# Kernel tuning notes

Measured on AMD Instinct MI355X. Metric: run time of the kernel, lower is better.

Reference implementation:

```python
import jax, jax.numpy as jnp
import numpy as np

HEADS = 4
ALPHA = 0.2
NEG = -9.0e15


def _layer(h, adj_mask, W, linW, linb, qkvW, qkvb, a, concat):
    # One GraphSelfAttentionLayer (eval mode: dropout off).
    F_out = W.shape[-1]
    n = h.shape[0]
    Wh = (h @ W) @ linW + linb                      # [N, F]
    qkv = Wh @ qkvW + qkvb                          # [N, 3F]
    q, k, v = jnp.split(qkv, 3, axis=-1)
    to_heads = lambda t: t.reshape(n, HEADS, F_out // HEADS).transpose(1, 0, 2)
    q, k, v = to_heads(q), to_heads(k), to_heads(v)  # [H, N, d]
    # note: scale uses out_features (not per-head d), matching the source
    dots = jax.nn.softmax(jnp.einsum('hid,hjd->hij', q, k) * (F_out ** -0.5), axis=-1)
    Wh0 = jnp.einsum('hij,hjd->hid', dots, v).transpose(1, 0, 2).reshape(n, F_out)
    Wh0 = jax.nn.softmax(Wh0, axis=-1)
    # decomposed all-pairs GAT score: e[i,j] = leakyrelu(Wh_i.a1 + Wh_j.a2)
    f1 = Wh @ a[:F_out]                             # [N]
    f2 = Wh @ a[F_out:]
    e = jax.nn.leaky_relu(f1[:, None] + f2[None, :], ALPHA)
    logits = jnp.where(adj_mask, e + dots.sum(0), NEG)
    att = jax.nn.softmax(logits, axis=1)
    hp = att @ Wh + Wh0
    return jax.nn.elu(hp) if concat else hp


def setup_inputs() -> dict:
    key = jax.random.key(0)
    ks = jax.random.split(key, 16)
    N, NFEAT, NHID, NOUT, H = 3072, 128, 32, 64, 4
    s = 0.1
    return {
        'x': jax.random.normal(ks[0], (N, NFEAT), jnp.float32),
        'adj': jax.random.randint(ks[1], (N, N), 0, 2, dtype=jnp.int32),
        'W_h': jax.random.normal(ks[2], (H, NFEAT, NHID), jnp.float32) * s,
        'lin_W_h': jax.random.normal(ks[3], (H, NHID, NHID), jnp.float32) * s,
        'lin_b_h': jax.random.normal(ks[4], (H, NHID), jnp.float32) * s,
        'qkv_W_h': jax.random.normal(ks[5], (H, NHID, 3 * NHID), jnp.float32) * s,
        'qkv_b_h': jax.random.normal(ks[6], (H, 3 * NHID), jnp.float32) * s,
        'a_h': jax.random.normal(ks[7], (H, 2 * NHID), jnp.float32) * s,
        'W_o': jax.random.normal(ks[8], (NHID * H, NOUT), jnp.float32) * s,
        'lin_W_o': jax.random.normal(ks[9], (NOUT, NOUT), jnp.float32) * s,
        'lin_b_o': jax.random.normal(ks[10], (NOUT,), jnp.float32) * s,
        'qkv_W_o': jax.random.normal(ks[11], (NOUT, 3 * NOUT), jnp.float32) * s,
        'qkv_b_o': jax.random.normal(ks[12], (3 * NOUT,), jnp.float32) * s,
        'a_o': jax.random.normal(ks[13], (2 * NOUT,), jnp.float32) * s,
    }


def reference(x, adj, W_h, lin_W_h, lin_b_h, qkv_W_h, qkv_b_h, a_h,
              W_o, lin_W_o, lin_b_o, qkv_W_o, qkv_b_o, a_o):
    mask = adj > 0
    heads_out = jax.vmap(
        lambda W, lW, lb, qW, qb, a: _layer(x, mask, W, lW, lb, qW, qb, a, True)
    )(W_h, lin_W_h, lin_b_h, qkv_W_h, qkv_b_h, a_h)      # [H, N, NHID]
    n = x.shape[0]
    x1 = jax.nn.elu(heads_out.transpose(1, 0, 2).reshape(n, -1))  # cat(dim=1) then elu
    out = jax.nn.elu(_layer(x1, mask, W_o, lin_W_o, lin_b_o, qkv_W_o, qkv_b_o, a_o, False))
    return out
```

## Files before the change

kernel.cpp:

```cpp
#include <hip/hip_runtime.h>
#include <hip/hip_bf16.h>

#define LOG2E 1.4426950408889634f
#define DEFER_THR 11.0f

typedef unsigned int u32;
typedef float f32x16 __attribute__((ext_vector_type(16)));
typedef short sh8 __attribute__((ext_vector_type(8)));

union FR { u32 u[4]; sh8 s; };

__device__ __forceinline__ u32 cvt_pk_bf16(float lo, float hi){
  u32 r;
  asm volatile("v_cvt_pk_bf16_f32 %0, %1, %2" : "=v"(r) : "v"(lo), "v"(hi));
  return r;
}

template<int W>
__device__ __forceinline__ float wred_max(float v){
  #pragma unroll
  for (int o=1;o<W;o<<=1) v = fmaxf(v, __shfl_xor(v,o));
  return v;
}
template<int W>
__device__ __forceinline__ float wred_sum(float v){
  #pragma unroll
  for (int o=1;o<W;o<<=1) v += __shfl_xor(v,o);
  return v;
}

__global__ __launch_bounds__(256) void k_mask(const int* __restrict__ adj, u32* __restrict__ mk){
  int id = blockIdx.x*256 + threadIdx.x;
  const int4* src = (const int4*)(adj + (size_t)id*32);
  u32 m = 0;
  #pragma unroll
  for (int g=0; g<8; g++){
    int4 v = src[g];
    if (v.x>0) m |= 1u<<(g*4+0);
    if (v.y>0) m |= 1u<<(g*4+1);
    if (v.z>0) m |= 1u<<(g*4+2);
    if (v.w>0) m |= 1u<<(g*4+3);
  }
  mk[id] = m;
}

template<int FIN, int F>
__global__ __launch_bounds__(256) void k_pre_a(const float* __restrict__ xg, const float* __restrict__ Wg,
    const float* __restrict__ lWg, const float* __restrict__ lbg, float* __restrict__ Whg, int N)
{
  const int h = blockIdx.y;
  const int row = blockIdx.x*256 + threadIdx.x;
  __shared__ float Wl[FIN*F];
  __shared__ float lWl[F*F];
  __shared__ float lbl[F];
  for (int i=threadIdx.x;i<FIN*F;i+=256) Wl[i]=Wg[(size_t)h*FIN*F+i];
  for (int i=threadIdx.x;i<F*F;i+=256) lWl[i]=lWg[(size_t)h*F*F+i];
  if (threadIdx.x<F) lbl[threadIdx.x]=lbg[h*F+threadIdx.x];
  __syncthreads();
  float t[F];
  #pragma unroll
  for (int c=0;c<F;c++) t[c]=0.f;
  const float4* xr = (const float4*)(xg + (size_t)row*FIN);
  for (int k4=0;k4<FIN/4;k4++){
    float4 xv = xr[k4];
    float xs[4]={xv.x,xv.y,xv.z,xv.w};
    #pragma unroll
    for (int kk=0;kk<4;kk++){
      float x1 = xs[kk];
      const float* wrow = Wl + (k4*4+kk)*F;
      #pragma unroll
      for (int c=0;c<F;c++) t[c] = fmaf(x1, wrow[c], t[c]);
    }
  }
  float wh[F];
  #pragma unroll
  for (int c=0;c<F;c++) wh[c]=lbl[c];
  #pragma unroll
  for (int k=0;k<F;k++){
    float tv=t[k];
    #pragma unroll
    for (int c=0;c<F;c++) wh[c]=fmaf(tv, lWl[k*F+c], wh[c]);
  }
  float4* dst=(float4*)(Whg + ((size_t)h*N+row)*F);
  #pragma unroll
  for (int c4=0;c4<F/4;c4++) dst[c4]=make_float4(wh[c4*4],wh[c4*4+1],wh[c4*4+2],wh[c4*4+3]);
}

template<int F, int GPR>
__global__ __launch_bounds__(256) void k_pre_b(const float* __restrict__ Whg, const float* __restrict__ qWg,
   const float* __restrict__ qbg, const float* __restrict__ ag,
   float* __restrict__ qg, float* __restrict__ kg, float* __restrict__ vg,
   float* __restrict__ f1g, float* __restrict__ f2g, int N)
{
  constexpr int ROWS = 256/GPR;
  constexpr int GC3  = 3*F/GPR;
  const int h = blockIdx.y;
  const int rl = threadIdx.x / GPR, grp = threadIdx.x % GPR;
  const int row = blockIdx.x*ROWS + rl;
  __shared__ float qWl[F*3*F];
  __shared__ float qbl[3*F];
  __shared__ float al[2*F];
  __shared__ float whl[ROWS][F+1];
  for (int i=threadIdx.x;i<F*3*F;i+=256) qWl[i]=qWg[(size_t)h*F*3*F+i];
  if (threadIdx.x<3*F) qbl[threadIdx.x]=qbg[h*3*F+threadIdx.x];
  if (threadIdx.x<2*F) al[threadIdx.x]=ag[h*2*F+threadIdx.x];
  {
    const float4* wsrc = (const float4*)(Whg + ((size_t)h*N+row)*F);
    #pragma unroll
    for (int c4=0;c4<2;c4++){
      float4 t = wsrc[grp*2+c4];
      int b = grp*8+c4*4;
      whl[rl][b]=t.x; whl[rl][b+1]=t.y; whl[rl][b+2]=t.z; whl[rl][b+3]=t.w;
    }
  }
  __syncthreads();
  float acc[GC3];
  #pragma unroll
  for (int c=0;c<GC3;c++) acc[c]=qbl[grp*GC3+c];
  for (int k=0;k<F;k++){
    float wv = whl[rl][k];
    #pragma unroll
    for (int c=0;c<GC3;c++) acc[c]=fmaf(wv, qWl[k*3*F + grp*GC3 + c], acc[c]);
  }
  size_t base = ((size_t)h*N+row)*F;
  #pragma unroll
  for (int c=0;c<GC3;c++){
    int col = grp*GC3+c;
    if (col < F)        qg[base+col]       = acc[c];
    else if (col < 2*F) kg[base+col-F]     = acc[c];
    else                vg[base+col-2*F]   = acc[c];
  }
  if (grp<2){
    const float* av = al + grp*F;
    float s=0.f;
    for (int k=0;k<F;k++) s = fmaf(whl[rl][k], av[k], s);
    (grp? f2g:f1g)[(size_t)h*N+row] = s;
  }
}

template<int S>
__global__ __launch_bounds__(256) void k_sweep1_mfma32(const float* __restrict__ qg, const float* __restrict__ kg,
    const float* __restrict__ vg, float* __restrict__ pml, float* __restrict__ pw, int N, float qscale)
{
  constexpr int F=32, LROW=33;
  const int h = blockIdx.z;
  const int sc = blockIdx.y;
  const int JC = N/S;
  const int wid = threadIdx.x>>6;
  const int lane = threadIdx.x&63;
  const int l31 = lane&31;
  const int half = lane>>5;
  const int itile = blockIdx.x*4 + wid;
  const int i = itile*32 + l31;
  __shared__ float kt[32*LROW];
  __shared__ float vt[32*LROW];

  sh8 qf[4];
  {
    const float* qrow = qg + ((size_t)h*N + i)*F;
    #pragma unroll
    for (int hh=0;hh<4;hh++){
      FR u;
      #pragma unroll
      for (int p=0;p<4;p++){
        float lo = half? 0.f : qrow[hh*8+2*p];
        float hi = half? 0.f : qrow[hh*8+2*p+1];
        u.u[p] = cvt_pk_bf16(lo,hi);
      }
      qf[hh]=u.s;
    }
  }
  f32x16 C;
  #pragma unroll
  for (int r=0;r<16;r++) C[r]=0.f;
  float m[4], l[4];
  #pragma unroll
  for (int hh=0;hh<4;hh++){ m[hh]=-1e30f; l[hh]=0.f; }
  const sh8 zf = {0,0,0,0,0,0,0,0};

  const int j0 = sc*JC;
  for (int jt=0; jt<JC; jt+=32){
    __syncthreads();
    {
      const float4* ks = (const float4*)(kg + ((size_t)h*N + j0+jt)*F);
      const float4* vs = (const float4*)(vg + ((size_t)h*N + j0+jt)*F);
      int idx = threadIdx.x;
      int j = idx>>3, c4 = idx&7;
      float4 a = ks[idx], b = vs[idx];
      float* kd = kt + j*LROW + c4*4;
      kd[0]=a.x; kd[1]=a.y; kd[2]=a.z; kd[3]=a.w;
      float* vd = vt + j*LROW + c4*4;
      vd[0]=b.x; vd[1]=b.y; vd[2]=b.z; vd[3]=b.w;
    }
    __syncthreads();
    sh8 vA[2];
    #pragma unroll
    for (int c=0;c<2;c++){
      FR u;
      #pragma unroll
      for (int p=0;p<4;p++){
        int jl = c*16 + half*8 + 2*p;
        u.u[p]=cvt_pk_bf16(vt[jl*LROW + l31], vt[(jl+1)*LROW + l31]);
      }
      vA[c]=u.s;
    }
    #pragma unroll
    for (int hh=0;hh<4;hh++){
      sh8 kf;
      {
        FR u;
        const float* kr = kt + l31*LROW + hh*8;
        #pragma unroll
        for (int p=0;p<4;p++){
          float lo = half? 0.f : kr[2*p];
          float hi = half? 0.f : kr[2*p+1];
          u.u[p]=cvt_pk_bf16(lo,hi);
        }
        kf=u.s;
      }
      f32x16 Sacc;
      #pragma unroll
      for (int r=0;r<16;r++) Sacc[r]=0.f;
      Sacc = __builtin_amdgcn_mfma_f32_32x32x16_bf16(kf, qf[hh], Sacc, 0,0,0);
      float mx = Sacc[0];
      #pragma unroll
      for (int r=1;r<16;r++) mx = fmaxf(mx, Sacc[r]);
      mx = fmaxf(mx, __shfl_xor(mx,32));
      mx *= qscale;
      float td = mx - m[hh];
      if (td > DEFER_THR){
        float corr = exp2f(-td);
        l[hh] *= corr;
        #pragma unroll
        for (int r=0;r<4;r++) C[hh*4+r] *= corr;
        m[hh] = mx;
      }
      float p[16];
      float ml = m[hh];
      float lsum=0.f;
      #pragma unroll
      for (int r=0;r<16;r++){ p[r] = exp2f(fmaf(Sacc[r], qscale, -ml)); lsum += p[r]; }
      l[hh] += lsum;
      const bool own = ((l31>>3)==hh);
      #pragma unroll
      for (int c=0;c<2;c++){
        u32 a01 = cvt_pk_bf16(p[c*8+0], p[c*8+1]);
        u32 a23 = cvt_pk_bf16(p[c*8+2], p[c*8+3]);
        u32 b01 = cvt_pk_bf16(p[c*8+4], p[c*8+5]);
        u32 b23 = cvt_pk_bf16(p[c*8+6], p[c*8+7]);
        u32 a01s = __shfl_xor(a01,32);
        u32 a23s = __shfl_xor(a23,32);
        u32 b01s = __shfl_xor(b01,32);
        u32 b23s = __shfl_xor(b23,32);
        FR bf;
        bf.u[0] = half? b01s : a01;
        bf.u[1] = half? b23s : a23;
        bf.u[2] = half? b01  : a01s;
        bf.u[3] = half? b23  : a23s;
        sh8 av = own ? vA[c] : zf;
        C = __builtin_amdgcn_mfma_f32_32x32x16_bf16(av, bf.s, C, 0,0,0);
      }
    }
  }
  float lt[4];
  #pragma unroll
  for (int hh=0;hh<4;hh++) lt[hh] = l[hh] + __shfl_xor(l[hh],32);
  if (half==0){
    float* pb = pml + ((size_t)(h*S+sc)*8)*N + i;
    #pragma unroll
    for (int hh=0;hh<4;hh++){ pb[(size_t)hh*N]=m[hh]; pb[(size_t)(4+hh)*N]=lt[hh]; }
  }
  {
    float* pv = pw + ((size_t)(h*S+sc)*N + i)*F;
    #pragma unroll
    for (int hh=0;hh<4;hh++){
      *(float4*)(pv + 8*hh + 4*half) = make_float4(C[hh*4],C[hh*4+1],C[hh*4+2],C[hh*4+3]);
    }
  }
}

template<int S>
__global__ __launch_bounds__(256) void k_sweep2_mfma32(const float* __restrict__ qg, const float* __restrict__ kg,
    const float* __restrict__ whg, const float* __restrict__ f1g, const float* __restrict__ f2g,
    const float* __restrict__ mstar, const float* __restrict__ invl, const u32* __restrict__ mk,
    float* __restrict__ p2ml, float* __restrict__ php, int N, float qscale)
{
  constexpr int F=32, LROW=33;
  const int h = blockIdx.z;
  const int sc = blockIdx.y;
  const int JC = N/S;
  const int wid = threadIdx.x>>6;
  const int lane = threadIdx.x&63;
  const int l31 = lane&31;
  const int half = lane>>5;
  const int itile = blockIdx.x*4 + wid;
  const int i = itile*32 + l31;
  const int nw = N>>5;
  __shared__ float kt[32*LROW];
  __shared__ float wt[32*LROW];
  __shared__ float f2s[32];

  sh8 qf[4];
  {
    const float* qrow = qg + ((size_t)h*N + i)*F;
    #pragma unroll
    for (int hh=0;hh<4;hh++){
      FR u;
      #pragma unroll
      for (int p=0;p<4;p++){
        float lo = half? 0.f : qrow[hh*8+2*p];
        float hi = half? 0.f : qrow[hh*8+2*p+1];
        u.u[p] = cvt_pk_bf16(lo,hi);
      }
      qf[hh]=u.s;
    }
  }
  float cc[4];
  #pragma unroll
  for (int hh=0;hh<4;hh++){
    float msv = mstar[((size_t)(h*4+hh))*N+i];
    float ilv = invl [((size_t)(h*4+hh))*N+i];
    cc[hh] = log2f(ilv) - msv;
  }
  const float f1 = f1g[(size_t)h*N+i];
  f32x16 C;
  #pragma unroll
  for (int r=0;r<16;r++) C[r]=0.f;
  float M=-1e30f, L=0.f;

  const int j0 = sc*JC;
  for (int jt=0; jt<JC; jt+=32){
    __syncthreads();
    {
      const float4* ks = (const float4*)(kg + ((size_t)h*N + j0+jt)*F);
      const float4* ws = (const float4*)(whg + ((size_t)h*N + j0+jt)*F);
      int idx = threadIdx.x;
      int j = idx>>3, c4 = idx&7;
      float4 a = ks[idx], b = ws[idx];
      float* kd = kt + j*LROW + c4*4;
      kd[0]=a.x; kd[1]=a.y; kd[2]=a.z; kd[3]=a.w;
      float* wd = wt + j*LROW + c4*4;
      wd[0]=b.x; wd[1]=b.y; wd[2]=b.z; wd[3]=b.w;
      if (threadIdx.x<32) f2s[threadIdx.x] = f2g[(size_t)h*N + j0+jt+threadIdx.x];
    }
    __syncthreads();
    float ds[16];
    #pragma unroll
    for (int r=0;r<16;r++) ds[r]=0.f;
    #pragma unroll
    for (int hh=0;hh<4;hh++){
      sh8 kf;
      {
        FR u;
        const float* kr = kt + l31*LROW + hh*8;
        #pragma unroll
        for (int p=0;p<4;p++){
          float lo = half? 0.f : kr[2*p];
          float hi = half? 0.f : kr[2*p+1];
          u.u[p]=cvt_pk_bf16(lo,hi);
        }
        kf=u.s;
      }
      f32x16 Sacc;
      #pragma unroll
      for (int r=0;r<16;r++) Sacc[r]=0.f;
      Sacc = __builtin_amdgcn_mfma_f32_32x32x16_bf16(kf, qf[hh], Sacc, 0,0,0);
      float ch = cc[hh];
      #pragma unroll
      for (int r=0;r<16;r++) ds[r] += exp2f(fmaf(Sacc[r], qscale, ch));
    }
    u32 mw = mk[(size_t)i*nw + ((j0+jt)>>5)];
    float w[16];
    float tm = -1e30f;
    #pragma unroll
    for (int r=0;r<16;r++){
      int jo = (r&3)+8*(r>>2)+4*half;
      float e = f1 + f2s[jo];
      e = (e>=0.f)? e : 0.2f*e;
      float lg = (e+ds[r])*LOG2E;
      w[r] = ((mw>>jo)&1u) ? lg : -1e30f;
      tm = fmaxf(tm, w[r]);
    }
    tm = fmaxf(tm, __shfl_xor(tm,32));
    float td = tm - M;
    if (td > DEFER_THR){
      float corr = exp2f(-td);
      L *= corr;
      #pragma unroll
      for (int r=0;r<16;r++) C[r] *= corr;
      M = tm;
    }
    float lsum=0.f;
    #pragma unroll
    for (int r=0;r<16;r++){
      float wv = (w[r] > -1e29f) ? exp2f(w[r]-M) : 0.f;
      w[r]=wv; lsum+=wv;
    }
    L += lsum;
    #pragma unroll
    for (int c=0;c<2;c++){
      sh8 whA;
      {
        FR u;
        #pragma unroll
        for (int p=0;p<4;p++){
          int jl = c*16 + half*8 + 2*p;
          u.u[p]=cvt_pk_bf16(wt[jl*LROW + l31], wt[(jl+1)*LROW + l31]);
        }
        whA=u.s;
      }
      u32 a01 = cvt_pk_bf16(w[c*8+0], w[c*8+1]);
      u32 a23 = cvt_pk_bf16(w[c*8+2], w[c*8+3]);
      u32 b01 = cvt_pk_bf16(w[c*8+4], w[c*8+5]);
      u32 b23 = cvt_pk_bf16(w[c*8+6], w[c*8+7]);
      u32 a01s = __shfl_xor(a01,32);
      u32 a23s = __shfl_xor(a23,32);
      u32 b01s = __shfl_xor(b01,32);
      u32 b23s = __shfl_xor(b23,32);
      FR bf;
      bf.u[0] = half? b01s : a01;
      bf.u[1] = half? b23s : a23;
      bf.u[2] = half? b01  : a01s;
      bf.u[3] = half? b23  : a23s;
      C = __builtin_amdgcn_mfma_f32_32x32x16_bf16(whA, bf.s, C, 0,0,0);
    }
  }
  L = L + __shfl_xor(L,32);
  if (half==0){
    float* pb = p2ml + ((size_t)(h*S+sc)*2)*N + i;
    pb[0]=M; pb[(size_t)N]=L;
  }
  {
    float* pv = php + ((size_t)(h*S+sc)*N + i)*F;
    #pragma unroll
    for (int g=0;g<4;g++)
      *(float4*)(pv + 8*g + 4*half) = make_float4(C[g*4],C[g*4+1],C[g*4+2],C[g*4+3]);
  }
}

template<int S>
__global__ __launch_bounds__(256) void k_sweep1_mfma64(const float* __restrict__ qg, const float* __restrict__ kg,
    const float* __restrict__ vg, float* __restrict__ pml, float* __restrict__ pw, int N, float qscale)
{
  constexpr int F=64, LROW=65;
  const int h = blockIdx.z;
  const int sc = blockIdx.y;
  const int JC = N/S;
  const int wid = threadIdx.x>>6;
  const int lane = threadIdx.x&63;
  const int l31 = lane&31;
  const int half = lane>>5;
  const int itile = blockIdx.x*4 + wid;
  const int i = itile*32 + l31;
  __shared__ float kt[32*LROW];
  __shared__ float vt[32*LROW];

  sh8 qf[4];
  {
    const float* qrow = qg + ((size_t)h*N + i)*F;
    #pragma unroll
    for (int hh=0;hh<4;hh++){
      FR u;
      #pragma unroll
      for (int p=0;p<4;p++)
        u.u[p] = cvt_pk_bf16(qrow[hh*16 + 8*half + 2*p], qrow[hh*16 + 8*half + 2*p+1]);
      qf[hh]=u.s;
    }
  }
  f32x16 C0, C1;
  #pragma unroll
  for (int r=0;r<16;r++){ C0[r]=0.f; C1[r]=0.f; }
  float m[4], l[4];
  #pragma unroll
  for (int hh=0;hh<4;hh++){ m[hh]=-1e30f; l[hh]=0.f; }
  const sh8 zf = {0,0,0,0,0,0,0,0};

  const int j0 = sc*JC;
  for (int jt=0; jt<JC; jt+=32){
    __syncthreads();
    {
      const float4* ks = (const float4*)(kg + ((size_t)h*N + j0+jt)*F);
      const float4* vs = (const float4*)(vg + ((size_t)h*N + j0+jt)*F);
      #pragma unroll
      for (int q2=0;q2<2;q2++){
        int idx = q2*256 + threadIdx.x;
        int j = idx>>4, c4 = idx&15;
        float4 a = ks[idx], b = vs[idx];
        float* kd = kt + j*LROW + c4*4;
        kd[0]=a.x; kd[1]=a.y; kd[2]=a.z; kd[3]=a.w;
        float* vd = vt + j*LROW + c4*4;
        vd[0]=b.x; vd[1]=b.y; vd[2]=b.z; vd[3]=b.w;
      }
    }
    __syncthreads();
    sh8 vA[2][2];
    #pragma unroll
    for (int ch=0;ch<2;ch++)
      #pragma unroll
      for (int c=0;c<2;c++){
        FR u;
        #pragma unroll
        for (int p=0;p<4;p++){
          int jl = c*16 + half*8 + 2*p;
          u.u[p]=cvt_pk_bf16(vt[jl*LROW + ch*32 + l31], vt[(jl+1)*LROW + ch*32 + l31]);
        }
        vA[ch][c]=u.s;
      }
    #pragma unroll
    for (int hh=0;hh<4;hh++){
      sh8 kf;
      {
        FR u;
        const float* kr = kt + l31*LROW + hh*16 + 8*half;
        #pragma unroll
        for (int p=0;p<4;p++) u.u[p]=cvt_pk_bf16(kr[2*p], kr[2*p+1]);
        kf=u.s;
      }
      f32x16 Sacc;
      #pragma unroll
      for (int r=0;r<16;r++) Sacc[r]=0.f;
      Sacc = __builtin_amdgcn_mfma_f32_32x32x16_bf16(kf, qf[hh], Sacc, 0,0,0);
      float mx = Sacc[0];
      #pragma unroll
      for (int r=1;r<16;r++) mx = fmaxf(mx, Sacc[r]);
      mx = fmaxf(mx, __shfl_xor(mx,32));
      mx *= qscale;
      f32x16 &Cr = (hh>>1)? C1 : C0;
      float td = mx - m[hh];
      if (td > DEFER_THR){
        float corr = exp2f(-td);
        l[hh] *= corr;
        if ((hh&1)==0){
          #pragma unroll
          for (int r=0;r<8;r++) Cr[r] *= corr;
        } else {
          #pragma unroll
          for (int r=8;r<16;r++) Cr[r] *= corr;
        }
        m[hh] = mx;
      }
      float p[16];
      float ml = m[hh];
      float lsum=0.f;
      #pragma unroll
      for (int r=0;r<16;r++){ p[r] = exp2f(fmaf(Sacc[r], qscale, -ml)); lsum += p[r]; }
      l[hh] += lsum;
      const bool own = ((l31>>4) == (hh&1));
      #pragma unroll
      for (int c=0;c<2;c++){
        u32 a01 = cvt_pk_bf16(p[c*8+0], p[c*8+1]);
        u32 a23 = cvt_pk_bf16(p[c*8+2], p[c*8+3]);
        u32 b01 = cvt_pk_bf16(p[c*8+4], p[c*8+5]);
        u32 b23 = cvt_pk_bf16(p[c*8+6], p[c*8+7]);
        u32 a01s = __shfl_xor(a01,32);
        u32 a23s = __shfl_xor(a23,32);
        u32 b01s = __shfl_xor(b01,32);
        u32 b23s = __shfl_xor(b23,32);
        FR bf;
        bf.u[0] = half? b01s : a01;
        bf.u[1] = half? b23s : a23;
        bf.u[2] = half? b01  : a01s;
        bf.u[3] = half? b23  : a23s;
        sh8 av = own ? vA[hh>>1][c] : zf;
        Cr = __builtin_amdgcn_mfma_f32_32x32x16_bf16(av, bf.s, Cr, 0,0,0);
      }
    }
  }
  float lt[4];
  #pragma unroll
  for (int hh=0;hh<4;hh++) lt[hh] = l[hh] + __shfl_xor(l[hh],32);
  if (half==0){
    float* pb = pml + ((size_t)(h*S+sc)*8)*N + i;
    #pragma unroll
    for (int hh=0;hh<4;hh++){ pb[(size_t)hh*N]=m[hh]; pb[(size_t)(4+hh)*N]=lt[hh]; }
  }
  {
    float* pv = pw + ((size_t)(h*S+sc)*N + i)*F;
    #pragma unroll
    for (int g=0;g<4;g++){
      *(float4*)(pv + 8*g + 4*half)      = make_float4(C0[g*4],C0[g*4+1],C0[g*4+2],C0[g*4+3]);
      *(float4*)(pv + 32 + 8*g + 4*half) = make_float4(C1[g*4],C1[g*4+1],C1[g*4+2],C1[g*4+3]);
    }
  }
}

template<int S>
__global__ __launch_bounds__(256) void k_sweep2_mfma64(const float* __restrict__ qg, const float* __restrict__ kg,
    const float* __restrict__ whg, const float* __restrict__ f1g, const float* __restrict__ f2g,
    const float* __restrict__ mstar, const float* __restrict__ invl, const u32* __restrict__ mk,
    float* __restrict__ p2ml, float* __restrict__ php, int N, float qscale)
{
  constexpr int F=64, LROW=65;
  const int h = blockIdx.z;
  const int sc = blockIdx.y;
  const int JC = N/S;
  const int wid = threadIdx.x>>6;
  const int lane = threadIdx.x&63;
  const int l31 = lane&31;
  const int half = lane>>5;
  const int itile = blockIdx.x*4 + wid;
  const int i = itile*32 + l31;
  const int nw = N>>5;
  __shared__ float kt[32*LROW];
  __shared__ float wt[32*LROW];
  __shared__ float f2s[32];

  sh8 qf[4];
  {
    const float* qrow = qg + ((size_t)h*N + i)*F;
    #pragma unroll
    for (int hh=0;hh<4;hh++){
      FR u;
      #pragma unroll
      for (int p=0;p<4;p++)
        u.u[p] = cvt_pk_bf16(qrow[hh*16 + 8*half + 2*p], qrow[hh*16 + 8*half + 2*p+1]);
      qf[hh]=u.s;
    }
  }
  float cc[4];
  #pragma unroll
  for (int hh=0;hh<4;hh++){
    float msv = mstar[((size_t)(h*4+hh))*N+i];
    float ilv = invl [((size_t)(h*4+hh))*N+i];
    cc[hh] = log2f(ilv) - msv;
  }
  const float f1 = f1g[(size_t)h*N+i];
  f32x16 C0, C1;
  #pragma unroll
  for (int r=0;r<16;r++){ C0[r]=0.f; C1[r]=0.f; }
  float M=-1e30f, L=0.f;

  const int j0 = sc*JC;
  for (int jt=0; jt<JC; jt+=32){
    __syncthreads();
    {
      const float4* ks = (const float4*)(kg + ((size_t)h*N + j0+jt)*F);
      const float4* ws = (const float4*)(whg + ((size_t)h*N + j0+jt)*F);
      #pragma unroll
      for (int q2=0;q2<2;q2++){
        int idx = q2*256 + threadIdx.x;
        int j = idx>>4, c4 = idx&15;
        float4 a = ks[idx], b = ws[idx];
        float* kd = kt + j*LROW + c4*4;
        kd[0]=a.x; kd[1]=a.y; kd[2]=a.z; kd[3]=a.w;
        float* wd = wt + j*LROW + c4*4;
        wd[0]=b.x; wd[1]=b.y; wd[2]=b.z; wd[3]=b.w;
      }
      if (threadIdx.x<32) f2s[threadIdx.x] = f2g[(size_t)h*N + j0+jt+threadIdx.x];
    }
    __syncthreads();
    float ds[16];
    #pragma unroll
    for (int r=0;r<16;r++) ds[r]=0.f;
    #pragma unroll
    for (int hh=0;hh<4;hh++){
      sh8 kf;
      {
        FR u;
        const float* kr = kt + l31*LROW + hh*16 + 8*half;
        #pragma unroll
        for (int p=0;p<4;p++) u.u[p]=cvt_pk_bf16(kr[2*p], kr[2*p+1]);
        kf=u.s;
      }
      f32x16 Sacc;
      #pragma unroll
      for (int r=0;r<16;r++) Sacc[r]=0.f;
      Sacc = __builtin_amdgcn_mfma_f32_32x32x16_bf16(kf, qf[hh], Sacc, 0,0,0);
      float ch = cc[hh];
      #pragma unroll
      for (int r=0;r<16;r++) ds[r] += exp2f(fmaf(Sacc[r], qscale, ch));
    }
    u32 mw = mk[(size_t)i*nw + ((j0+jt)>>5)];
    float w[16];
    float tm = -1e30f;
    #pragma unroll
    for (int r=0;r<16;r++){
      int jo = (r&3)+8*(r>>2)+4*half;
      float e = f1 + f2s[jo];
      e = (e>=0.f)? e : 0.2f*e;
      float lg = (e+ds[r])*LOG2E;
      w[r] = ((mw>>jo)&1u) ? lg : -1e30f;
      tm = fmaxf(tm, w[r]);
    }
    tm = fmaxf(tm, __shfl_xor(tm,32));
    float td = tm - M;
    if (td > DEFER_THR){
      float corr = exp2f(-td);
      L *= corr;
      #pragma unroll
      for (int r=0;r<16;r++){ C0[r] *= corr; C1[r] *= corr; }
      M = tm;
    }
    float lsum=0.f;
    #pragma unroll
    for (int r=0;r<16;r++){
      float wv = (w[r] > -1e29f) ? exp2f(w[r]-M) : 0.f;
      w[r]=wv; lsum+=wv;
    }
    L += lsum;
    #pragma unroll
    for (int c=0;c<2;c++){
      u32 a01 = cvt_pk_bf16(w[c*8+0], w[c*8+1]);
      u32 a23 = cvt_pk_bf16(w[c*8+2], w[c*8+3]);
      u32 b01 = cvt_pk_bf16(w[c*8+4], w[c*8+5]);
      u32 b23 = cvt_pk_bf16(w[c*8+6], w[c*8+7]);
      u32 a01s = __shfl_xor(a01,32);
      u32 a23s = __shfl_xor(a23,32);
      u32 b01s = __shfl_xor(b01,32);
      u32 b23s = __shfl_xor(b23,32);
      FR bf;
      bf.u[0] = half? b01s : a01;
      bf.u[1] = half? b23s : a23;
      bf.u[2] = half? b01  : a01s;
      bf.u[3] = half? b23  : a23s;
      #pragma unroll
      for (int ch=0;ch<2;ch++){
        sh8 whA;
        {
          FR u;
          #pragma unroll
          for (int p=0;p<4;p++){
            int jl = c*16 + half*8 + 2*p;
            u.u[p]=cvt_pk_bf16(wt[jl*LROW + ch*32 + l31], wt[(jl+1)*LROW + ch*32 + l31]);
          }
          whA=u.s;
        }
        if (ch) C1 = __builtin_amdgcn_mfma_f32_32x32x16_bf16(whA, bf.s, C1, 0,0,0);
        else    C0 = __builtin_amdgcn_mfma_f32_32x32x16_bf16(whA, bf.s, C0, 0,0,0);
      }
    }
  }
  L = L + __shfl_xor(L,32);
  if (half==0){
    float* pb = p2ml + ((size_t)(h*S+sc)*2)*N + i;
    pb[0]=M; pb[(size_t)N]=L;
  }
  {
    float* pv = php + ((size_t)(h*S+sc)*N + i)*F;
    #pragma unroll
    for (int g=0;g<4;g++){
      *(float4*)(pv + 8*g + 4*half)      = make_float4(C0[g*4],C0[g*4+1],C0[g*4+2],C0[g*4+3]);
      *(float4*)(pv + 32 + 8*g + 4*half) = make_float4(C1[g*4],C1[g*4+1],C1[g*4+2],C1[g*4+3]);
    }
  }
}

template<int S>
__global__ __launch_bounds__(256) void k_stats1(const float* __restrict__ pml, float* __restrict__ wgt1,
    float* __restrict__ mstar, float* __restrict__ invl, int N)
{
  const int h = blockIdx.y>>2, hh = blockIdx.y&3;
  const int row = blockIdx.x*256 + threadIdx.x;
  float mv[S];
  #pragma unroll
  for (int sc=0;sc<S;sc++) mv[sc]=pml[((size_t)((h*S+sc)*8)+hh)*N+row];
  float ms=-1e30f;
  #pragma unroll
  for (int sc=0;sc<S;sc++) ms=fmaxf(ms,mv[sc]);
  float ls=0.f;
  #pragma unroll
  for (int sc=0;sc<S;sc++){
    float w = exp2f(mv[sc]-ms);
    float lv = pml[((size_t)((h*S+sc)*8)+4+hh)*N+row];
    ls = fmaf(lv, w, ls);
    wgt1[((size_t)((h*S+sc)*4)+hh)*N+row]=w;
  }
  mstar[((size_t)(h*4+hh))*N+row]=ms;
  invl [((size_t)(h*4+hh))*N+row]=1.f/ls;
}

template<int F, int S>
__global__ __launch_bounds__(256) void k_comb1(const float* __restrict__ pw, const float* __restrict__ wgt1,
    const float* __restrict__ invl, float* __restrict__ smw, int N)
{
  constexpr int D = F/4;
  constexpr int RPB = 256/F;
  const int h = blockIdx.y;
  const int c = threadIdx.x % F;
  const int row = blockIdx.x*RPB + threadIdx.x / F;
  const int hh = c / D;
  float acc=0.f;
  #pragma unroll
  for (int sc=0;sc<S;sc++){
    float w = wgt1[((size_t)((h*S+sc)*4)+hh)*N+row];
    float p = pw[((size_t)(h*S+sc)*N + row)*F + c];
    acc = fmaf(w,p,acc);
  }
  float w0 = acc * invl[((size_t)(h*4+hh))*N+row];
  float mx = wred_max<F>(w0);
  float e = exp2f((w0-mx)*LOG2E);
  float sm = wred_sum<F>(e);
  smw[((size_t)h*N+row)*F + c] = e/sm;
}

template<int S>
__global__ __launch_bounds__(256) void k_stats2(const float* __restrict__ p2ml, float* __restrict__ wgt2,
    float* __restrict__ invL, int N)
{
  const int h = blockIdx.y;
  const int row = blockIdx.x*256 + threadIdx.x;
  float mv[S];
  #pragma unroll
  for (int sc=0;sc<S;sc++) mv[sc]=p2ml[((size_t)((h*S+sc)*2))*N+row];
  float M=-1e30f;
  #pragma unroll
  for (int sc=0;sc<S;sc++) M=fmaxf(M,mv[sc]);
  float L=0.f;
  #pragma unroll
  for (int sc=0;sc<S;sc++){
    float w=exp2f(mv[sc]-M);
    float lv=p2ml[((size_t)((h*S+sc)*2)+1)*N+row];
    L = fmaf(lv,w,L);
    wgt2[(size_t)(h*S+sc)*N+row]=w;
  }
  invL[(size_t)h*N+row]=1.f/L;
}

template<int F, int S, bool L1OUT>
__global__ __launch_bounds__(256) void k_comb2(const float* __restrict__ php, const float* __restrict__ wgt2,
    const float* __restrict__ invL, const float* __restrict__ smw, void* __restrict__ outp, int N)
{
  constexpr int RPB = 256/F;
  const int h = blockIdx.y;
  const int c = threadIdx.x % F;
  const int row = blockIdx.x*RPB + threadIdx.x / F;
  float acc=0.f;
  #pragma unroll
  for (int sc=0;sc<S;sc++){
    float w = wgt2[(size_t)(h*S+sc)*N+row];
    float p = php[((size_t)(h*S+sc)*N + row)*F + c];
    acc = fmaf(w,p,acc);
  }
  float v = acc * invL[(size_t)h*N+row] + smw[((size_t)h*N+row)*F + c];
  v = (v>0.f)? v : expm1f(v);
  if (L1OUT){
    v = (v>0.f)? v : expm1f(v);
    ((float*)outp)[(size_t)row*(4*F) + h*F + c] = v;
  } else {
    ((float*)outp)[(size_t)row*F + c] = v;
  }
}

extern "C" void kernel_launch(void* const* d_in, const int* in_sizes, int n_in,
                              void* d_out, int out_size, void* d_ws, size_t ws_size,
                              hipStream_t stream)
{
  (void)in_sizes; (void)n_in; (void)out_size; (void)ws_size;
  const int N=3072;
  const int S1=16, S2=32;

  const float* x      = (const float*)d_in[0];
  const int*   adj    = (const int*)d_in[1];
  const float* W_h    = (const float*)d_in[2];
  const float* linW_h = (const float*)d_in[3];
  const float* linb_h = (const float*)d_in[4];
  const float* qkvW_h = (const float*)d_in[5];
  const float* qkvb_h = (const float*)d_in[6];
  const float* a_h    = (const float*)d_in[7];
  const float* W_o    = (const float*)d_in[8];
  const float* linW_o = (const float*)d_in[9];
  const float* linb_o = (const float*)d_in[10];
  const float* qkvW_o = (const float*)d_in[11];
  const float* qkvb_o = (const float*)d_in[12];
  const float* a_o    = (const float*)d_in[13];

  char* w = (char*)d_ws;
  auto alloc=[&](size_t bytes)->char*{ char* p=w; w += (bytes+255)&~(size_t)255; return p; };
  u32*   mk    = (u32*)  alloc((size_t)N*(N/32)*4);
  float* Wh1   = (float*)alloc((size_t)4*N*32*4);
  float* q1    = (float*)alloc((size_t)4*N*32*4);
  float* k1    = (float*)alloc((size_t)4*N*32*4);
  float* v1    = (float*)alloc((size_t)4*N*32*4);
  float* f11   = (float*)alloc((size_t)4*N*4);
  float* f21   = (float*)alloc((size_t)4*N*4);
  float* smw1  = (float*)alloc((size_t)4*32*N*4);
  float* x1    = (float*)alloc((size_t)N*128*4);
  float* Wh2   = (float*)alloc((size_t)N*64*4);
  float* q2    = (float*)alloc((size_t)N*64*4);
  float* k2    = (float*)alloc((size_t)N*64*4);
  float* v2    = (float*)alloc((size_t)N*64*4);
  float* f12   = (float*)alloc((size_t)N*4);
  float* f22   = (float*)alloc((size_t)N*4);
  float* smw2  = (float*)alloc((size_t)64*N*4);
  float* mst   = (float*)alloc((size_t)16*N*4);
  float* ivl   = (float*)alloc((size_t)16*N*4);
  float* wgt1  = (float*)alloc((size_t)256*N*4);
  float* wgt2  = (float*)alloc((size_t)64*N*4);
  float* ivL   = (float*)alloc((size_t)4*N*4);
  float* pml   = (float*)alloc((size_t)512*N*4);
  float* pw    = (float*)alloc((size_t)2048*N*4);

  const float qs1 = 0.17677669529663687f * LOG2E;
  const float qs2 = 0.125f * LOG2E;

  k_mask<<<dim3(N*(N/32)/256), 256, 0, stream>>>(adj, mk);

  k_pre_a<128,32><<<dim3(N/256,4),256,0,stream>>>(x, W_h, linW_h, linb_h, Wh1, N);
  k_pre_b<32,4><<<dim3(N/64,4),256,0,stream>>>(Wh1, qkvW_h, qkvb_h, a_h, q1,k1,v1,f11,f21,N);
  k_sweep1_mfma32<16><<<dim3(N/128,16,4),256,0,stream>>>(q1,k1,v1,pml,pw,N,qs1);
  k_stats1<16><<<dim3(N/256,16),256,0,stream>>>(pml,wgt1,mst,ivl,N);
  k_comb1<32,16><<<dim3(N/8,4),256,0,stream>>>(pw,wgt1,ivl,smw1,N);
  k_sweep2_mfma32<16><<<dim3(N/128,16,4),256,0,stream>>>(q1,k1,Wh1,f11,f21,mst,ivl,mk,pml,pw,N,qs1);
  k_stats2<16><<<dim3(N/256,4),256,0,stream>>>(pml,wgt2,ivL,N);
  k_comb2<32,16,true><<<dim3(N/8,4),256,0,stream>>>(pw,wgt2,ivL,smw1,x1,N);

  k_pre_a<128,64><<<dim3(N/256,1),256,0,stream>>>(x1, W_o, linW_o, linb_o, Wh2, N);
  k_pre_b<64,8><<<dim3(N/32,1),256,0,stream>>>(Wh2, qkvW_o, qkvb_o, a_o, q2,k2,v2,f12,f22,N);
  k_sweep1_mfma64<32><<<dim3(N/128,S2,1),256,0,stream>>>(q2,k2,v2,pml,pw,N,qs2);
  k_stats1<32><<<dim3(N/256,4),256,0,stream>>>(pml,wgt1,mst,ivl,N);
  k_comb1<64,32><<<dim3(N/4,1),256,0,stream>>>(pw,wgt1,ivl,smw2,N);
  k_sweep2_mfma64<32><<<dim3(N/128,S2,1),256,0,stream>>>(q2,k2,Wh2,f12,f22,mst,ivl,mk,pml,pw,N,qs2);
  k_stats2<32><<<dim3(N/256,1),256,0,stream>>>(pml,wgt2,ivL,N);
  k_comb2<64,32,false><<<dim3(N/4,1),256,0,stream>>>(pw,wgt2,ivL,smw2,d_out,N);
}
```

Measured before the change: 418.6 us.

## Load K fragments directly from global memory and halve layer-1 split count

Drops the LDS staging of K tiles in all four sweep kernels; each lane now loads its K row directly from global with float4 loads and converts to bf16. It also removes the masked-value branch in the exp computation by starting M at -1e29, and reduces the layer-1 j-split from 16 to 8, which shrinks the partial-stat buffers. The aim is to cut LDS traffic, shared-memory stores and per-split reduction overhead. The cost is uncached-in-LDS global reads of K and fewer blocks in flight for layer 1. In the 32-wide kernels, lanes that used to zero their K inputs now load real data, so correctness depends on the zeroed Q half cancelling those terms.

```diff
diff --git a/kernel.cpp b/kernel.cpp
--- a/kernel.cpp
+++ b/kernel.cpp
@@ -152,7 +152,6 @@
   const int half = lane>>5;
   const int itile = blockIdx.x*4 + wid;
   const int i = itile*32 + l31;
-  __shared__ float kt[32*LROW];
   __shared__ float vt[32*LROW];
 
   sh8 qf[4];
@@ -182,17 +181,15 @@
   for (int jt=0; jt<JC; jt+=32){
     __syncthreads();
     {
-      const float4* ks = (const float4*)(kg + ((size_t)h*N + j0+jt)*F);
       const float4* vs = (const float4*)(vg + ((size_t)h*N + j0+jt)*F);
       int idx = threadIdx.x;
       int j = idx>>3, c4 = idx&7;
-      float4 a = ks[idx], b = vs[idx];
-      float* kd = kt + j*LROW + c4*4;
-      kd[0]=a.x; kd[1]=a.y; kd[2]=a.z; kd[3]=a.w;
+      float4 b = vs[idx];
       float* vd = vt + j*LROW + c4*4;
       vd[0]=b.x; vd[1]=b.y; vd[2]=b.z; vd[3]=b.w;
     }
     __syncthreads();
+    const float* krow = kg + ((size_t)h*N + j0+jt + l31)*F;
     sh8 vA[2];
     #pragma unroll
     for (int c=0;c<2;c++){
@@ -209,13 +206,12 @@
       sh8 kf;
       {
         FR u;
-        const float* kr = kt + l31*LROW + hh*8;
-        #pragma unroll
-        for (int p=0;p<4;p++){
-          float lo = half? 0.f : kr[2*p];
-          float hi = half? 0.f : kr[2*p+1];
-          u.u[p]=cvt_pk_bf16(lo,hi);
-        }
+        float4 ka = *(const float4*)(krow + hh*8);
+        float4 kb = *(const float4*)(krow + hh*8 + 4);
+        u.u[0]=cvt_pk_bf16(ka.x,ka.y);
+        u.u[1]=cvt_pk_bf16(ka.z,ka.w);
+        u.u[2]=cvt_pk_bf16(kb.x,kb.y);
+        u.u[3]=cvt_pk_bf16(kb.z,kb.w);
         kf=u.s;
       }
       f32x16 Sacc;
@@ -296,7 +292,6 @@
   const int itile = blockIdx.x*4 + wid;
   const int i = itile*32 + l31;
   const int nw = N>>5;
-  __shared__ float kt[32*LROW];
   __shared__ float wt[32*LROW];
   __shared__ float f2s[32];
 
@@ -326,24 +321,22 @@
   f32x16 C;
   #pragma unroll
   for (int r=0;r<16;r++) C[r]=0.f;
-  float M=-1e30f, L=0.f;
+  float M=-1e29f, L=0.f;
 
   const int j0 = sc*JC;
   for (int jt=0; jt<JC; jt+=32){
     __syncthreads();
     {
-      const float4* ks = (const float4*)(kg + ((size_t)h*N + j0+jt)*F);
       const float4* ws = (const float4*)(whg + ((size_t)h*N + j0+jt)*F);
       int idx = threadIdx.x;
       int j = idx>>3, c4 = idx&7;
-      float4 a = ks[idx], b = ws[idx];
-      float* kd = kt + j*LROW + c4*4;
-      kd[0]=a.x; kd[1]=a.y; kd[2]=a.z; kd[3]=a.w;
+      float4 b = ws[idx];
       float* wd = wt + j*LROW + c4*4;
       wd[0]=b.x; wd[1]=b.y; wd[2]=b.z; wd[3]=b.w;
       if (threadIdx.x<32) f2s[threadIdx.x] = f2g[(size_t)h*N + j0+jt+threadIdx.x];
     }
     __syncthreads();
+    const float* krow = kg + ((size_t)h*N + j0+jt + l31)*F;
     float ds[16];
     #pragma unroll
     for (int r=0;r<16;r++) ds[r]=0.f;
@@ -352,13 +345,12 @@
       sh8 kf;
       {
         FR u;
-        const float* kr = kt + l31*LROW + hh*8;
-        #pragma unroll
-        for (int p=0;p<4;p++){
-          float lo = half? 0.f : kr[2*p];
-          float hi = half? 0.f : kr[2*p+1];
-          u.u[p]=cvt_pk_bf16(lo,hi);
-        }
+        float4 ka = *(const float4*)(krow + hh*8);
+        float4 kb = *(const float4*)(krow + hh*8 + 4);
+        u.u[0]=cvt_pk_bf16(ka.x,ka.y);
+        u.u[1]=cvt_pk_bf16(ka.z,ka.w);
+        u.u[2]=cvt_pk_bf16(kb.x,kb.y);
+        u.u[3]=cvt_pk_bf16(kb.z,kb.w);
         kf=u.s;
       }
       f32x16 Sacc;
@@ -393,7 +385,7 @@
     float lsum=0.f;
     #pragma unroll
     for (int r=0;r<16;r++){
-      float wv = (w[r] > -1e29f) ? exp2f(w[r]-M) : 0.f;
+      float wv = exp2f(w[r]-M);
       w[r]=wv; lsum+=wv;
     }
     L += lsum;
@@ -452,7 +444,6 @@
   const int half = lane>>5;
   const int itile = blockIdx.x*4 + wid;
   const int i = itile*32 + l31;
-  __shared__ float kt[32*LROW];
   __shared__ float vt[32*LROW];
 
   sh8 qf[4];
@@ -479,20 +470,18 @@
   for (int jt=0; jt<JC; jt+=32){
     __syncthreads();
     {
-      const float4* ks = (const float4*)(kg + ((size_t)h*N + j0+jt)*F);
       const float4* vs = (const float4*)(vg + ((size_t)h*N + j0+jt)*F);
       #pragma unroll
       for (int q2=0;q2<2;q2++){
         int idx = q2*256 + threadIdx.x;
         int j = idx>>4, c4 = idx&15;
-        float4 a = ks[idx], b = vs[idx];
-        float* kd = kt + j*LROW + c4*4;
-        kd[0]=a.x; kd[1]=a.y; kd[2]=a.z; kd[3]=a.w;
+        float4 b = vs[idx];
         float* vd = vt + j*LROW + c4*4;
         vd[0]=b.x; vd[1]=b.y; vd[2]=b.z; vd[3]=b.w;
       }
     }
     __syncthreads();
+    const float* krow = kg + ((size_t)h*N + j0+jt + l31)*F;
     sh8 vA[2][2];
     #pragma unroll
     for (int ch=0;ch<2;ch++)
@@ -511,9 +500,12 @@
       sh8 kf;
       {
         FR u;
-        const float* kr = kt + l31*LROW + hh*16 + 8*half;
-        #pragma unroll
-        for (int p=0;p<4;p++) u.u[p]=cvt_pk_bf16(kr[2*p], kr[2*p+1]);
+        float4 ka = *(const float4*)(krow + hh*16 + 8*half);
+        float4 kb = *(const float4*)(krow + hh*16 + 8*half + 4);
+        u.u[0]=cvt_pk_bf16(ka.x,ka.y);
+        u.u[1]=cvt_pk_bf16(ka.z,ka.w);
+        u.u[2]=cvt_pk_bf16(kb.x,kb.y);
+        u.u[3]=cvt_pk_bf16(kb.z,kb.w);
         kf=u.s;
       }
       f32x16 Sacc;
@@ -601,7 +593,6 @@
   const int itile = blockIdx.x*4 + wid;
   const int i = itile*32 + l31;
   const int nw = N>>5;
-  __shared__ float kt[32*LROW];
   __shared__ float wt[32*LROW];
   __shared__ float f2s[32];
 
@@ -628,27 +619,25 @@
   f32x16 C0, C1;
   #pragma unroll
   for (int r=0;r<16;r++){ C0[r]=0.f; C1[r]=0.f; }
-  float M=-1e30f, L=0.f;
+  float M=-1e29f, L=0.f;
 
   const int j0 = sc*JC;
   for (int jt=0; jt<JC; jt+=32){
     __syncthreads();
     {
-      const float4* ks = (const float4*)(kg + ((size_t)h*N + j0+jt)*F);
       const float4* ws = (const float4*)(whg + ((size_t)h*N + j0+jt)*F);
       #pragma unroll
       for (int q2=0;q2<2;q2++){
         int idx = q2*256 + threadIdx.x;
         int j = idx>>4, c4 = idx&15;
-        float4 a = ks[idx], b = ws[idx];
-        float* kd = kt + j*LROW + c4*4;
-        kd[0]=a.x; kd[1]=a.y; kd[2]=a.z; kd[3]=a.w;
+        float4 b = ws[idx];
         float* wd = wt + j*LROW + c4*4;
         wd[0]=b.x; wd[1]=b.y; wd[2]=b.z; wd[3]=b.w;
       }
       if (threadIdx.x<32) f2s[threadIdx.x] = f2g[(size_t)h*N + j0+jt+threadIdx.x];
     }
     __syncthreads();
+    const float* krow = kg + ((size_t)h*N + j0+jt + l31)*F;
     float ds[16];
     #pragma unroll
     for (int r=0;r<16;r++) ds[r]=0.f;
@@ -657,9 +646,12 @@
       sh8 kf;
       {
         FR u;
-        const float* kr = kt + l31*LROW + hh*16 + 8*half;
-        #pragma unroll
-        for (int p=0;p<4;p++) u.u[p]=cvt_pk_bf16(kr[2*p], kr[2*p+1]);
+        float4 ka = *(const float4*)(krow + hh*16 + 8*half);
+        float4 kb = *(const float4*)(krow + hh*16 + 8*half + 4);
+        u.u[0]=cvt_pk_bf16(ka.x,ka.y);
+        u.u[1]=cvt_pk_bf16(ka.z,ka.w);
+        u.u[2]=cvt_pk_bf16(kb.x,kb.y);
+        u.u[3]=cvt_pk_bf16(kb.z,kb.w);
         kf=u.s;
       }
       f32x16 Sacc;
@@ -694,7 +686,7 @@
     float lsum=0.f;
     #pragma unroll
     for (int r=0;r<16;r++){
-      float wv = (w[r] > -1e29f) ? exp2f(w[r]-M) : 0.f;
+      float wv = exp2f(w[r]-M);
       w[r]=wv; lsum+=wv;
     }
     L += lsum;
@@ -847,7 +839,7 @@
 {
   (void)in_sizes; (void)n_in; (void)out_size; (void)ws_size;
   const int N=3072;
-  const int S1=16, S2=32;
+  const int S1=8, S2=32;
 
   const float* x      = (const float*)d_in[0];
   const int*   adj    = (const int*)d_in[1];
@@ -884,10 +876,10 @@
   float* smw2  = (float*)alloc((size_t)64*N*4);
   float* mst   = (float*)alloc((size_t)16*N*4);
   float* ivl   = (float*)alloc((size_t)16*N*4);
-  float* wgt1  = (float*)alloc((size_t)256*N*4);
-  float* wgt2  = (float*)alloc((size_t)64*N*4);
+  float* wgt1  = (float*)alloc((size_t)128*N*4);
+  float* wgt2  = (float*)alloc((size_t)32*N*4);
   float* ivL   = (float*)alloc((size_t)4*N*4);
-  float* pml   = (float*)alloc((size_t)512*N*4);
+  float* pml   = (float*)alloc((size_t)256*N*4);
   float* pw    = (float*)alloc((size_t)2048*N*4);
 
   const float qs1 = 0.17677669529663687f * LOG2E;
@@ -897,12 +889,12 @@
 
   k_pre_a<128,32><<<dim3(N/256,4),256,0,stream>>>(x, W_h, linW_h, linb_h, Wh1, N);
   k_pre_b<32,4><<<dim3(N/64,4),256,0,stream>>>(Wh1, qkvW_h, qkvb_h, a_h, q1,k1,v1,f11,f21,N);
-  k_sweep1_mfma32<16><<<dim3(N/128,16,4),256,0,stream>>>(q1,k1,v1,pml,pw,N,qs1);
-  k_stats1<16><<<dim3(N/256,16),256,0,stream>>>(pml,wgt1,mst,ivl,N);
-  k_comb1<32,16><<<dim3(N/8,4),256,0,stream>>>(pw,wgt1,ivl,smw1,N);
-  k_sweep2_mfma32<16><<<dim3(N/128,16,4),256,0,stream>>>(q1,k1,Wh1,f11,f21,mst,ivl,mk,pml,pw,N,qs1);
-  k_stats2<16><<<dim3(N/256,4),256,0,stream>>>(pml,wgt2,ivL,N);
-  k_comb2<32,16,true><<<dim3(N/8,4),256,0,stream>>>(pw,wgt2,ivL,smw1,x1,N);
+  k_sweep1_mfma32<8><<<dim3(N/128,8,4),256,0,stream>>>(q1,k1,v1,pml,pw,N,qs1);
+  k_stats1<8><<<dim3(N/256,16),256,0,stream>>>(pml,wgt1,mst,ivl,N);
+  k_comb1<32,8><<<dim3(N/8,4),256,0,stream>>>(pw,wgt1,ivl,smw1,N);
+  k_sweep2_mfma32<8><<<dim3(N/128,8,4),256,0,stream>>>(q1,k1,Wh1,f11,f21,mst,ivl,mk,pml,pw,N,qs1);
+  k_stats2<8><<<dim3(N/256,4),256,0,stream>>>(pml,wgt2,ivL,N);
+  k_comb2<32,8,true><<<dim3(N/8,4),256,0,stream>>>(pw,wgt2,ivL,smw1,x1,N);
 
   k_pre_a<128,64><<<dim3(N/256,1),256,0,stream>>>(x1, W_o, linW_o, linb_o, Wh2, N);
   k_pre_b<64,8><<<dim3(N/32,1),256,0,stream>>>(Wh2, qkvW_o, qkvb_o, a_o, q2,k2,v2,f12,f22,N);
```

After: 392.5 us. 6.2% less time.
